# Optimization experiments

Measured on AMD Instinct MI355X. Metric: run time of the kernel, lower is better.

The kernel has to match this reference:

```python
import jax, jax.numpy as jnp
import numpy as np

GROUPS = 4
EPS = 1e-5


def setup_inputs() -> dict:
    key = jax.random.key(0)
    k1, k2 = jax.random.split(key)
    x = jax.random.normal(k1, (8, 8, 64, 64, 64), dtype=jnp.float32)
    # ConvTranspose3d weight layout: [Cin, Cout, K, K, K]
    w = jax.random.normal(k2, (8, 16, 3, 3, 3), dtype=jnp.float32) * 0.1
    gamma = jnp.ones((16,), dtype=jnp.float32)
    beta = jnp.zeros((16,), dtype=jnp.float32)
    return {"x": x, "w": w, "gamma": gamma, "beta": beta}


def _conv_transpose3d_k3_s1_p0(x, w):
    # fp16 round-trip mimics the kernel's fp16 weight packing (math done in fp32)
    w16 = w.astype(jnp.float16).astype(jnp.float32)
    # transposed conv (k=3, s=1, p=0) == full conv with spatially flipped kernel
    wk = jnp.flip(w16, axis=(2, 3, 4)).transpose(1, 0, 2, 3, 4)  # [Cout,Cin,3,3,3]
    return jax.lax.conv_general_dilated(
        x, wk,
        window_strides=(1, 1, 1),
        padding=[(2, 2), (2, 2), (2, 2)],
        dimension_numbers=("NCDHW", "OIDHW", "NCDHW"),
    )


def reference(x, w, gamma, beta):
    y = _conv_transpose3d_k3_s1_p0(x, w)        # [N,Cout,66,66,66]
    r = jax.nn.relu(y)
    N, C = r.shape[0], r.shape[1]
    rg = r.reshape(N, GROUPS, -1)               # [N,G,(C/G)*D*H*W]
    mean = rg.mean(axis=2, keepdims=True)
    var = rg.var(axis=2, keepdims=True)
    norm = ((rg - mean) * jax.lax.rsqrt(var + EPS)).reshape(r.shape)
    g = gamma[None, :, None, None, None]
    b = beta[None, :, None, None, None]
    return norm * g + b
```

## Files before the change

### kernel.cpp

```cpp
#include <hip/hip_runtime.h>

#define N_BATCH 8
#define CI 8
#define CO 16
#define ODIM 66
#define OSP (66*66*66)
#define GROUPS 4

typedef _Float16 half8 __attribute__((ext_vector_type(8)));
typedef float f32x4 __attribute__((ext_vector_type(4)));

#define OHT 8
#define NWAVES 3
#define TPW 11
#define NTHR 192
#define XIH 10
#define XIW 68
#define PLPOS (XIH*XIW)
#define PLH (PLPOS*8)
#define RING 4
#define LOD 6
#define NODC 11
#define WSZ (28*16*8)
#define XPLANE 262144

__global__ __launch_bounds__(64) void zero_stats(float* ws) {
    ws[threadIdx.x] = 0.0f;
}

__device__ __forceinline__ void stage_issue(
    const float* __restrict__ x, size_t nbase, int id, int oh0, int tid,
    float xr[4][8], int sp[4], bool sok[4])
{
    #pragma unroll
    for (int it = 0; it < 4; ++it) {
        int p   = tid + it * NTHR;
        int ihl = p / XIW;
        int iw  = p - ihl * XIW - 2;
        int ih  = oh0 - 2 + ihl;
        bool ok = (p < PLPOS) & ((unsigned)id < 64u) &
                  ((unsigned)ih < 64u) & ((unsigned)iw < 64u);
        size_t base = nbase + (ok ? ((size_t)id * 4096 + (size_t)(ih * 64 + iw)) : 0);
        #pragma unroll
        for (int ci = 0; ci < 8; ++ci)
            xr[it][ci] = x[base + (size_t)ci * XPLANE];
        sp[it] = p; sok[it] = ok;
    }
}

__device__ __forceinline__ void stage_write(
    _Float16* XT, int slot, const float xr[4][8], const int sp[4], const bool sok[4])
{
    #pragma unroll
    for (int it = 0; it < 4; ++it) {
        if (sp[it] < PLPOS) {
            half8 h;
            #pragma unroll
            for (int ci = 0; ci < 8; ++ci)
                h[ci] = sok[it] ? (_Float16)xr[it][ci] : (_Float16)0.0f;
            *(half8*)&XT[slot * PLH + sp[it] * 8] = h;
        }
    }
}

__global__ __launch_bounds__(NTHR, 2) void conv_mfma(
    const float* __restrict__ x, const float* __restrict__ w,
    float* __restrict__ out, float* __restrict__ stats)
{
    __shared__ _Float16 XT[RING * PLH];
    __shared__ _Float16 WT[WSZ];
    __shared__ float reds[2][NWAVES][GROUPS];

    const int tid = threadIdx.x;
    const int n   = blockIdx.z;
    const int od0 = blockIdx.y * LOD;
    const int oh0 = blockIdx.x * OHT;

    for (int i = tid; i < 28 * 16; i += NTHR) {
        int t = i >> 4, co = i & 15;
        half8 h;
        #pragma unroll
        for (int ci = 0; ci < 8; ++ci) {
            float v = (t < 27) ? w[(ci * 16 + co) * 27 + t] : 0.0f;
            h[ci] = (_Float16)v;
        }
        *(half8*)&WT[i * 8] = h;
    }

    const size_t nbase = (size_t)(n * CI) * XPLANE;

    {
        float xr[4][8]; int sp[4]; bool sok[4];
        #pragma unroll
        for (int j = 0; j < 3; ++j) {
            stage_issue(x, nbase, od0 - 2 + j, oh0, tid, xr, sp, sok);
            stage_write(XT, j, xr, sp, sok);
        }
    }
    __syncthreads();

    const int lane = tid & 63;
    const int wv   = tid >> 6;
    const int q    = lane >> 4;
    const int col  = lane & 15;

    half8 bfrag[7];
    int sub[7], kd2[7];
    #pragma unroll
    for (int c = 0; c < 7; ++c) {
        int t = c * 4 + q;
        bfrag[c] = *(const half8*)&WT[(t * 16 + col) * 8];
        if (t > 26) t = 26;
        int kd = t / 9, r = t - kd * 9, kh = r / 3, kw = r - kh * 3;
        sub[c] = (kh * XIW + kw) * 8;
        kd2[c] = 2 - kd;
    }

    int basein[TPW];
    #pragma unroll
    for (int i = 0; i < TPW; ++i) {
        int p   = (wv * TPW + i) * 16 + col;
        int ohl = p / 66, ow = p - ohl * 66;
        basein[i] = ((ohl + 2) * XIW + (ow + 2)) * 8;
    }

    float s = 0.0f, ss = 0.0f;
    const int co = col;
    float* slab0 = out + (size_t)(n * CO + co) * OSP + (size_t)od0 * 4356 + oh0 * 66;

    float xr[4][8]; int sp[4]; bool sok[4];

    for (int k = 0; k < LOD; ++k) {
        const bool stg = (k < LOD - 1);
        if (stg) stage_issue(x, nbase, od0 + k + 1, oh0, tid, xr, sp, sok);

        f32x4 acc[TPW];
        #pragma unroll
        for (int i = 0; i < TPW; ++i) acc[i] = (f32x4){0.f, 0.f, 0.f, 0.f};

        int aoffc[7];
        #pragma unroll
        for (int c = 0; c < 7; ++c)
            aoffc[c] = ((k + kd2[c]) & 3) * PLH - sub[c];

        #pragma unroll
        for (int c = 0; c < 7; ++c) {
            #pragma unroll
            for (int i = 0; i < TPW; ++i) {
                half8 a = *(const half8*)&XT[basein[i] + aoffc[c]];
                acc[i] = __builtin_amdgcn_mfma_f32_16x16x32_f16(a, bfrag[c], acc[i], 0, 0, 0);
            }
        }

        float* slab = slab0 + (size_t)k * 4356;
        #pragma unroll
        for (int i = 0; i < TPW; ++i) {
            #pragma unroll
            for (int r = 0; r < 4; ++r) {
                int p   = (wv * TPW + i) * 16 + q * 4 + r;
                int ohl = p / 66, ow = p - ohl * 66;
                if (oh0 + ohl < ODIM) {
                    float v = fmaxf(acc[i][r], 0.0f);
                    slab[ohl * 66 + ow] = v;
                    s += v;
                    ss = fmaf(v, v, ss);
                }
            }
        }

        if (stg) stage_write(XT, (k + 3) & 3, xr, sp, sok);
        __syncthreads();
    }

    s += __shfl_xor(s, 16, 64);  ss += __shfl_xor(ss, 16, 64);
    s += __shfl_xor(s, 32, 64);  ss += __shfl_xor(ss, 32, 64);
    s += __shfl_xor(s, 1, 64);   ss += __shfl_xor(ss, 1, 64);
    s += __shfl_xor(s, 2, 64);   ss += __shfl_xor(ss, 2, 64);
    if (lane < 16 && (lane & 3) == 0) {
        reds[0][wv][lane >> 2] = s;
        reds[1][wv][lane >> 2] = ss;
    }
    __syncthreads();
    if (tid < GROUPS) {
        float ts = 0.0f, tss = 0.0f;
        #pragma unroll
        for (int v = 0; v < NWAVES; ++v) { ts += reds[0][v][tid]; tss += reds[1][v][tid]; }
        atomicAdd(&stats[n * GROUPS + tid], ts);
        atomicAdd(&stats[32 + n * GROUPS + tid], tss);
    }
}

#define NORM_ITER 8
#define NORM_NTHR 256
__global__ __launch_bounds__(NORM_NTHR) void norm_kernel(
    float* __restrict__ out, const float* __restrict__ ws,
    const float* __restrict__ gamma, const float* __restrict__ beta)
{
    const int slab = blockIdx.y;
    const int n  = slab >> 4;
    const int co = slab & 15;
    const int gi = n * GROUPS + (co >> 2);
    const float cnt  = 4.0f * (float)OSP;
    const float mean = ws[gi] / cnt;
    const float var  = ws[32 + gi] / cnt - mean * mean;
    const float rstd = rsqrtf(var + 1e-5f);
    const float scale = rstd * gamma[co];
    const float shift = beta[co] - mean * scale;

    float4* p = (float4*)(out + (size_t)slab * OSP);
    const int base = blockIdx.x * (NORM_NTHR * NORM_ITER) + threadIdx.x;
    #pragma unroll
    for (int it = 0; it < NORM_ITER; ++it) {
        const int idx = base + it * NORM_NTHR;
        if (idx < OSP / 4) {
            float4 v = p[idx];
            v.x = fmaf(v.x, scale, shift);
            v.y = fmaf(v.y, scale, shift);
            v.z = fmaf(v.z, scale, shift);
            v.w = fmaf(v.w, scale, shift);
            p[idx] = v;
        }
    }
}

extern "C" void kernel_launch(void* const* d_in, const int* in_sizes, int n_in,
                              void* d_out, int out_size, void* d_ws, size_t ws_size,
                              hipStream_t stream) {
    const float* x     = (const float*)d_in[0];
    const float* w     = (const float*)d_in[1];
    const float* gamma = (const float*)d_in[2];
    const float* beta  = (const float*)d_in[3];
    float* out = (float*)d_out;
    float* ws  = (float*)d_ws;

    zero_stats<<<1, 64, 0, stream>>>(ws);

    dim3 grid1((ODIM + OHT - 1) / OHT, NODC, N_BATCH);
    conv_mfma<<<grid1, NTHR, 0, stream>>>(x, w, out, ws);

    const int f4_per_slab = OSP / 4;
    dim3 grid2((f4_per_slab + NORM_NTHR * NORM_ITER - 1) / (NORM_NTHR * NORM_ITER),
               N_BATCH * CO);
    norm_kernel<<<grid2, NORM_NTHR, 0, stream>>>(out, ws, gamma, beta);
}
```

Baseline: 336.3 us.

## Shrink LDS ring to three slots, vectorize staging loads, raise occupancy

The input-plane ring buffer in LDS drops from four slots to three, which frees shared memory so launch bounds can request three blocks per CU instead of two. Staging now loads float2 pairs along W, halving the number of global load instructions and per-thread staging registers. Because a three-slot ring reuses the slot just read, an extra barrier is placed before each stage write, and full __syncthreads are replaced with lgkmcnt-wait plus s_barrier. The depth loop is also fully unrolled so the modulo-3 slot indices become constants. The extra barrier per iteration and the tighter register budget may offset the occupancy gain.

```diff
diff --git a/kernel.cpp b/kernel.cpp
--- a/kernel.cpp
+++ b/kernel.cpp
@@ -17,53 +17,61 @@
 #define XIH 10
 #define XIW 68
 #define PLPOS (XIH*XIW)
+#define PLPAIR (PLPOS/2)
 #define PLH (PLPOS*8)
-#define RING 4
+#define RING 3
 #define LOD 6
 #define NODC 11
 #define WSZ (28*16*8)
 #define XPLANE 262144
 
+#define LGKM_BARRIER() asm volatile("s_waitcnt lgkmcnt(0)\n\ts_barrier" ::: "memory")
+
 __global__ __launch_bounds__(64) void zero_stats(float* ws) {
     ws[threadIdx.x] = 0.0f;
 }
 
 __device__ __forceinline__ void stage_issue(
     const float* __restrict__ x, size_t nbase, int id, int oh0, int tid,
-    float xr[4][8], int sp[4], bool sok[4])
-{
-    #pragma unroll
-    for (int it = 0; it < 4; ++it) {
-        int p   = tid + it * NTHR;
-        int ihl = p / XIW;
-        int iw  = p - ihl * XIW - 2;
-        int ih  = oh0 - 2 + ihl;
-        bool ok = (p < PLPOS) & ((unsigned)id < 64u) &
-                  ((unsigned)ih < 64u) & ((unsigned)iw < 64u);
-        size_t base = nbase + (ok ? ((size_t)id * 4096 + (size_t)(ih * 64 + iw)) : 0);
+    float2 xr[2][8], int sp[2], bool sok[2])
+{
+    #pragma unroll
+    for (int it = 0; it < 2; ++it) {
+        int p2  = tid + it * NTHR;
+        int row = p2 / 34;
+        int u   = p2 - row * 34;
+        int iw0 = 2 * u - 2;
+        int ih  = oh0 - 2 + row;
+        bool ok = (p2 < PLPAIR) & ((unsigned)id < 64u) &
+                  ((unsigned)ih < 64u) & ((unsigned)iw0 < 63u);
+        size_t base = nbase + (ok ? ((size_t)id * 4096 + (size_t)(ih * 64 + iw0)) : 0);
         #pragma unroll
         for (int ci = 0; ci < 8; ++ci)
-            xr[it][ci] = x[base + (size_t)ci * XPLANE];
-        sp[it] = p; sok[it] = ok;
+            xr[it][ci] = *(const float2*)&x[base + (size_t)ci * XPLANE];
+        sp[it] = p2; sok[it] = ok;
     }
 }
 
 __device__ __forceinline__ void stage_write(
-    _Float16* XT, int slot, const float xr[4][8], const int sp[4], const bool sok[4])
-{
-    #pragma unroll
-    for (int it = 0; it < 4; ++it) {
-        if (sp[it] < PLPOS) {
-            half8 h;
+    _Float16* XT, int slot, const float2 xr[2][8], const int sp[2], const bool sok[2])
+{
+    #pragma unroll
+    for (int it = 0; it < 2; ++it) {
+        if (sp[it] < PLPAIR) {
+            half8 h0, h1;
             #pragma unroll
-            for (int ci = 0; ci < 8; ++ci)
-                h[ci] = sok[it] ? (_Float16)xr[it][ci] : (_Float16)0.0f;
-            *(half8*)&XT[slot * PLH + sp[it] * 8] = h;
-        }
-    }
-}
-
-__global__ __launch_bounds__(NTHR, 2) void conv_mfma(
+            for (int ci = 0; ci < 8; ++ci) {
+                h0[ci] = sok[it] ? (_Float16)xr[it][ci].x : (_Float16)0.0f;
+                h1[ci] = sok[it] ? (_Float16)xr[it][ci].y : (_Float16)0.0f;
+            }
+            _Float16* dst = &XT[slot * PLH + sp[it] * 16];
+            *(half8*)dst = h0;
+            *(half8*)(dst + 8) = h1;
+        }
+    }
+}
+
+__global__ __launch_bounds__(NTHR, 3) void conv_mfma(
     const float* __restrict__ x, const float* __restrict__ w,
     float* __restrict__ out, float* __restrict__ stats)
 {
@@ -90,14 +98,14 @@
     const size_t nbase = (size_t)(n * CI) * XPLANE;
 
     {
-        float xr[4][8]; int sp[4]; bool sok[4];
+        float2 xr[2][8]; int sp[2]; bool sok[2];
         #pragma unroll
         for (int j = 0; j < 3; ++j) {
             stage_issue(x, nbase, od0 - 2 + j, oh0, tid, xr, sp, sok);
             stage_write(XT, j, xr, sp, sok);
         }
     }
-    __syncthreads();
+    LGKM_BARRIER();
 
     const int lane = tid & 63;
     const int wv   = tid >> 6;
@@ -105,7 +113,7 @@
     const int col  = lane & 15;
 
     half8 bfrag[7];
-    int sub[7], kd2[7];
+    int sub[7], kdc[7];
     #pragma unroll
     for (int c = 0; c < 7; ++c) {
         int t = c * 4 + q;
@@ -113,7 +121,7 @@
         if (t > 26) t = 26;
         int kd = t / 9, r = t - kd * 9, kh = r / 3, kw = r - kh * 3;
         sub[c] = (kh * XIW + kw) * 8;
-        kd2[c] = 2 - kd;
+        kdc[c] = 2 - kd;
     }
 
     int basein[TPW];
@@ -128,8 +136,9 @@
     const int co = col;
     float* slab0 = out + (size_t)(n * CO + co) * OSP + (size_t)od0 * 4356 + oh0 * 66;
 
-    float xr[4][8]; int sp[4]; bool sok[4];
-
+    float2 xr[2][8]; int sp[2]; bool sok[2];
+
+    #pragma unroll
     for (int k = 0; k < LOD; ++k) {
         const bool stg = (k < LOD - 1);
         if (stg) stage_issue(x, nbase, od0 + k + 1, oh0, tid, xr, sp, sok);
@@ -141,7 +150,7 @@
         int aoffc[7];
         #pragma unroll
         for (int c = 0; c < 7; ++c)
-            aoffc[c] = ((k + kd2[c]) & 3) * PLH - sub[c];
+            aoffc[c] = ((k + kdc[c]) % 3) * PLH - sub[c];
 
         #pragma unroll
         for (int c = 0; c < 7; ++c) {
@@ -168,8 +177,11 @@
             }
         }
 
-        if (stg) stage_write(XT, (k + 3) & 3, xr, sp, sok);
-        __syncthreads();
+        if (stg) {
+            LGKM_BARRIER();
+            stage_write(XT, k % 3, xr, sp, sok);
+            LGKM_BARRIER();
+        }
     }
 
     s += __shfl_xor(s, 16, 64);  ss += __shfl_xor(ss, 16, 64);
```

New measurement: 482.1 us. +43.4%, slower.
